# Performance work log

Measured on AMD Instinct MI355X. Metric: run time of the kernel, lower is better.

## Reference

```python
import jax, jax.numpy as jnp
import numpy as np


def setup_inputs() -> dict:
    key = jax.random.key(0)
    k1, k2, k3 = jax.random.split(key, 3)
    return {
        "x": jax.random.normal(k1, (1, 64, 28, 28), dtype=jnp.float32),
        "w1": jax.random.normal(k2, (128, 32, 3, 3, 2), dtype=jnp.float32),  # weights[0]
        "w2": jax.random.normal(k3, (64, 3, 2), dtype=jnp.float32),          # weights[1]
    }


def reference(x, w1, w2):
    # Stage 1: first unfold + einsum == depthwise size-3 conv along W (pad 1),
    # producing 2 taps (k) per channel.
    xr = x.reshape(64, 28, 28)                      # (j, m=H, n=W)
    xp = jnp.pad(xr, ((0, 0), (0, 0), (1, 1)))      # zero-pad W by 1
    # t3[j, m, i, n] = xp[j, m, n + i]  (i = kernel offset 0..2)
    t3 = jnp.stack([xp[:, :, i:i + 28] for i in range(3)], axis=2)  # (64,28,3,28)
    t4 = jnp.einsum('jmin,jik->jmnk', t3, w2)       # (64,28,28,2)

    # Stage 2: pairwise channel-sum 64 -> 32
    t5 = t4.reshape(32, 2, 28, 28, 2).sum(axis=1)   # (l=32, h=28, w=28, k=2)

    # Stage 3: the two remaining unfolds + final einsum == standard 3x3 conv,
    # pad 1, in_channels = (l,k) = 64, out_channels = 128.
    inp = jnp.transpose(t5, (0, 3, 1, 2)).reshape(1, 64, 28, 28)       # NCHW, C=(l,k)
    w = jnp.transpose(w1, (0, 1, 4, 2, 3)).reshape(128, 64, 3, 3)      # OIHW, I=(l,m)
    y = jax.lax.conv_general_dilated(
        inp, w, window_strides=(1, 1), padding=((1, 1), (1, 1)),
        dimension_numbers=('NCHW', 'OIHW', 'NCHW'))
    return y  # (1, 128, 28, 28)
```

## Files before the change

kernel.cpp:

```cpp
#include <hip/hip_runtime.h>
#include <hip/hip_bf16.h>

__global__ __launch_bounds__(256, 2) void fused_kernel(
    const float* __restrict__ x,
    const float* __restrict__ w1,
    const float* __restrict__ w2,
    float* __restrict__ y)
{
    __shared__ __align__(16) float sA[64 * 220];

    const int b     = blockIdx.x;
    const int opair = b / 7;
    const int band  = b % 7;
    const int tid   = threadIdx.x;

    const int l8      = tid & 7;
    const int strip   = tid >> 3;
    const bool act    = (strip < 28);
    const int sclp    = act ? strip : 0;
    const int oo      = sclp / 14;
    const int rem     = sclp % 14;
    const int rp      = rem / 7;
    const int st      = rem % 7;
    const int o       = opair * 2 + oo;

    float2 wreg[4][9];
    {
        const float* wb = w1 + o * 576 + l8 * 18;
        #pragma unroll
        for (int li = 0; li < 4; ++li)
            #pragma unroll
            for (int t = 0; t < 9; ++t)
                wreg[li][t] = *(const float2*)(wb + li * 144 + t * 2);
    }

    if (tid < 192) {
        const int l  = tid / 6;
        const int pr = tid % 6;
        const int m  = band * 4 + pr - 1;
        const int j0 = 2 * l;
        float* dst0 = &sA[(2 * l)     * 220 + pr * 36];
        float* dst1 = &sA[(2 * l + 1) * 220 + pr * 36];
        if (m < 0 || m > 27) {
            #pragma unroll
            for (int t = 0; t < 7; ++t) {
                ((float4*)dst0)[t] = make_float4(0.f, 0.f, 0.f, 0.f);
                ((float4*)dst1)[t] = make_float4(0.f, 0.f, 0.f, 0.f);
            }
            ((float2*)dst0)[14] = make_float2(0.f, 0.f);
            ((float2*)dst1)[14] = make_float2(0.f, 0.f);
        } else {
            const float* xr0 = x + (j0 * 28 + m) * 28;
            const float* xr1 = xr0 + 28 * 28;
            const float2 a0 = *(const float2*)(w2 + j0 * 6 + 0);
            const float2 a1 = *(const float2*)(w2 + j0 * 6 + 2);
            const float2 a2 = *(const float2*)(w2 + j0 * 6 + 4);
            const float2 b0 = *(const float2*)(w2 + j0 * 6 + 6);
            const float2 b1 = *(const float2*)(w2 + j0 * 6 + 8);
            const float2 b2 = *(const float2*)(w2 + j0 * 6 + 10);

            float4 pv0 = make_float4(0.f, 0.f, 0.f, 0.f);
            float4 pv1 = make_float4(0.f, 0.f, 0.f, 0.f);
            #pragma unroll
            for (int t = 0; t < 7; ++t) {
                float4 v0 = ((const float4*)xr0)[t];
                float4 v1 = ((const float4*)xr1)[t];
                float4 o0, o1;
                o0.x = a0.x * pv0.z + a1.x * pv0.w + a2.x * v0.x
                     + b0.x * pv1.z + b1.x * pv1.w + b2.x * v1.x;
                o0.y = a0.x * pv0.w + a1.x * v0.x + a2.x * v0.y
                     + b0.x * pv1.w + b1.x * v1.x + b2.x * v1.y;
                o0.z = a0.x * v0.x + a1.x * v0.y + a2.x * v0.z
                     + b0.x * v1.x + b1.x * v1.y + b2.x * v1.z;
                o0.w = a0.x * v0.y + a1.x * v0.z + a2.x * v0.w
                     + b0.x * v1.y + b1.x * v1.z + b2.x * v1.w;
                o1.x = a0.y * pv0.z + a1.y * pv0.w + a2.y * v0.x
                     + b0.y * pv1.z + b1.y * pv1.w + b2.y * v1.x;
                o1.y = a0.y * pv0.w + a1.y * v0.x + a2.y * v0.y
                     + b0.y * pv1.w + b1.y * v1.x + b2.y * v1.y;
                o1.z = a0.y * v0.x + a1.y * v0.y + a2.y * v0.z
                     + b0.y * v1.x + b1.y * v1.y + b2.y * v1.z;
                o1.w = a0.y * v0.y + a1.y * v0.z + a2.y * v0.w
                     + b0.y * v1.y + b1.y * v1.z + b2.y * v1.w;
                if (t == 0) { o0.x = 0.f; o1.x = 0.f; }
                ((float4*)dst0)[t] = o0;
                ((float4*)dst1)[t] = o1;
                pv0 = v0; pv1 = v1;
            }
            float t28_0 = a0.x * pv0.z + a1.x * pv0.w
                        + b0.x * pv1.z + b1.x * pv1.w;
            float t28_1 = a0.y * pv0.z + a1.y * pv0.w
                        + b0.y * pv1.z + b1.y * pv1.w;
            ((float2*)dst0)[14] = make_float2(t28_0, 0.f);
            ((float2*)dst1)[14] = make_float2(t28_1, 0.f);
        }
    }
    __syncthreads();

    float acc00 = 0.f, acc01 = 0.f, acc02 = 0.f, acc03 = 0.f;
    float acc10 = 0.f, acc11 = 0.f, acc12 = 0.f, acc13 = 0.f;

    #pragma unroll
    for (int li = 0; li < 4; ++li) {
        #pragma unroll
        for (int ch = 0; ch < 2; ++ch) {
            const int c = (l8 + li * 8) * 2 + ch;
            const float* sa = &sA[c * 220 + (rp * 2) * 36 + st * 4];
            #pragma unroll
            for (int q = 0; q < 4; ++q) {
                float4 t0 = *(const float4*)(sa + q * 36);
                float2 t1 = *(const float2*)(sa + q * 36 + 4);
                if (q < 3) {
                    float2 W0 = wreg[li][q * 3 + 0];
                    float2 W1 = wreg[li][q * 3 + 1];
                    float2 W2 = wreg[li][q * 3 + 2];
                    float wa  = ch ? W0.y : W0.x;
                    float wbv = ch ? W1.y : W1.x;
                    float wc  = ch ? W2.y : W2.x;
                    acc00 += wa * t0.x + wbv * t0.y + wc * t0.z;
                    acc01 += wa * t0.y + wbv * t0.z + wc * t0.w;
                    acc02 += wa * t0.z + wbv * t0.w + wc * t1.x;
                    acc03 += wa * t0.w + wbv * t1.x + wc * t1.y;
                }
                if (q >= 1) {
                    float2 W0 = wreg[li][(q - 1) * 3 + 0];
                    float2 W1 = wreg[li][(q - 1) * 3 + 1];
                    float2 W2 = wreg[li][(q - 1) * 3 + 2];
                    float wa  = ch ? W0.y : W0.x;
                    float wbv = ch ? W1.y : W1.x;
                    float wc  = ch ? W2.y : W2.x;
                    acc10 += wa * t0.x + wbv * t0.y + wc * t0.z;
                    acc11 += wa * t0.y + wbv * t0.z + wc * t0.w;
                    acc12 += wa * t0.z + wbv * t0.w + wc * t1.x;
                    acc13 += wa * t0.w + wbv * t1.x + wc * t1.y;
                }
            }
        }
    }

    #pragma unroll
    for (int m = 1; m <= 4; m <<= 1) {
        acc00 += __shfl_xor(acc00, m); acc01 += __shfl_xor(acc01, m);
        acc02 += __shfl_xor(acc02, m); acc03 += __shfl_xor(acc03, m);
        acc10 += __shfl_xor(acc10, m); acc11 += __shfl_xor(acc11, m);
        acc12 += __shfl_xor(acc12, m); acc13 += __shfl_xor(acc13, m);
    }

    if (act && l8 == 0) {
        const int R0 = band * 4 + rp * 2;
        float* yp = y + (o * 28 + R0) * 28 + st * 4;
        *(float4*)yp        = make_float4(acc00, acc01, acc02, acc03);
        *(float4*)(yp + 28) = make_float4(acc10, acc11, acc12, acc13);
    }
}

extern "C" void kernel_launch(void* const* d_in, const int* in_sizes, int n_in,
                              void* d_out, int out_size, void* d_ws, size_t ws_size,
                              hipStream_t stream) {
    const float* x  = (const float*)d_in[0];
    const float* w1 = (const float*)d_in[1];
    const float* w2 = (const float*)d_in[2];
    float* yout = (float*)d_out;

    fused_kernel<<<dim3(448), dim3(256), 0, stream>>>(x, w1, w2, yout);
}
```

Measured before the change: 13.99 us.

## Interleave channel pairs in shared memory and pack accumulators as float2

Stage-1 output now goes to shared memory with the two k-taps of each channel pair interleaved, using one 372-float slab per pair instead of two 220-float slabs. The conv loop loads three float4 per row to cover both channels and accumulates into float2 pairs, which allows packed FMA and halves the number of LDS instructions per row. Shared memory per block drops, and launch bounds are raised to 3 blocks per CU for more occupancy. The trade-off is more register pressure under the tighter bound and different bank access patterns.

```diff
diff --git a/kernel.cpp b/kernel.cpp
--- a/kernel.cpp
+++ b/kernel.cpp
@@ -1,13 +1,13 @@
 #include <hip/hip_runtime.h>
 #include <hip/hip_bf16.h>
 
-__global__ __launch_bounds__(256, 2) void fused_kernel(
+__global__ __launch_bounds__(256, 3) void fused_kernel(
     const float* __restrict__ x,
     const float* __restrict__ w1,
     const float* __restrict__ w2,
     float* __restrict__ y)
 {
-    __shared__ __align__(16) float sA[64 * 220];
+    __shared__ __align__(16) float sB[32 * 372];
 
     const int b     = blockIdx.x;
     const int opair = b / 7;
@@ -39,16 +39,11 @@
         const int pr = tid % 6;
         const int m  = band * 4 + pr - 1;
         const int j0 = 2 * l;
-        float* dst0 = &sA[(2 * l)     * 220 + pr * 36];
-        float* dst1 = &sA[(2 * l + 1) * 220 + pr * 36];
+        float* dst = &sB[l * 372 + pr * 60];
         if (m < 0 || m > 27) {
             #pragma unroll
-            for (int t = 0; t < 7; ++t) {
-                ((float4*)dst0)[t] = make_float4(0.f, 0.f, 0.f, 0.f);
-                ((float4*)dst1)[t] = make_float4(0.f, 0.f, 0.f, 0.f);
-            }
-            ((float2*)dst0)[14] = make_float2(0.f, 0.f);
-            ((float2*)dst1)[14] = make_float2(0.f, 0.f);
+            for (int t = 0; t < 15; ++t)
+                ((float4*)dst)[t] = make_float4(0.f, 0.f, 0.f, 0.f);
         } else {
             const float* xr0 = x + (j0 * 28 + m) * 28;
             const float* xr1 = xr0 + 28 * 28;
@@ -65,78 +60,86 @@
             for (int t = 0; t < 7; ++t) {
                 float4 v0 = ((const float4*)xr0)[t];
                 float4 v1 = ((const float4*)xr1)[t];
-                float4 o0, o1;
-                o0.x = a0.x * pv0.z + a1.x * pv0.w + a2.x * v0.x
-                     + b0.x * pv1.z + b1.x * pv1.w + b2.x * v1.x;
-                o0.y = a0.x * pv0.w + a1.x * v0.x + a2.x * v0.y
-                     + b0.x * pv1.w + b1.x * v1.x + b2.x * v1.y;
-                o0.z = a0.x * v0.x + a1.x * v0.y + a2.x * v0.z
-                     + b0.x * v1.x + b1.x * v1.y + b2.x * v1.z;
-                o0.w = a0.x * v0.y + a1.x * v0.z + a2.x * v0.w
-                     + b0.x * v1.y + b1.x * v1.z + b2.x * v1.w;
-                o1.x = a0.y * pv0.z + a1.y * pv0.w + a2.y * v0.x
-                     + b0.y * pv1.z + b1.y * pv1.w + b2.y * v1.x;
-                o1.y = a0.y * pv0.w + a1.y * v0.x + a2.y * v0.y
-                     + b0.y * pv1.w + b1.y * v1.x + b2.y * v1.y;
-                o1.z = a0.y * v0.x + a1.y * v0.y + a2.y * v0.z
-                     + b0.y * v1.x + b1.y * v1.y + b2.y * v1.z;
-                o1.w = a0.y * v0.y + a1.y * v0.z + a2.y * v0.w
-                     + b0.y * v1.y + b1.y * v1.z + b2.y * v1.w;
-                if (t == 0) { o0.x = 0.f; o1.x = 0.f; }
-                ((float4*)dst0)[t] = o0;
-                ((float4*)dst1)[t] = o1;
+                float o0x = a0.x*pv0.z + a1.x*pv0.w + a2.x*v0.x
+                          + b0.x*pv1.z + b1.x*pv1.w + b2.x*v1.x;
+                float o1x = a0.y*pv0.z + a1.y*pv0.w + a2.y*v0.x
+                          + b0.y*pv1.z + b1.y*pv1.w + b2.y*v1.x;
+                float o0y = a0.x*pv0.w + a1.x*v0.x + a2.x*v0.y
+                          + b0.x*pv1.w + b1.x*v1.x + b2.x*v1.y;
+                float o1y = a0.y*pv0.w + a1.y*v0.x + a2.y*v0.y
+                          + b0.y*pv1.w + b1.y*v1.x + b2.y*v1.y;
+                float o0z = a0.x*v0.x + a1.x*v0.y + a2.x*v0.z
+                          + b0.x*v1.x + b1.x*v1.y + b2.x*v1.z;
+                float o1z = a0.y*v0.x + a1.y*v0.y + a2.y*v0.z
+                          + b0.y*v1.x + b1.y*v1.y + b2.y*v1.z;
+                float o0w = a0.x*v0.y + a1.x*v0.z + a2.x*v0.w
+                          + b0.x*v1.y + b1.x*v1.z + b2.x*v1.w;
+                float o1w = a0.y*v0.y + a1.y*v0.z + a2.y*v0.w
+                          + b0.y*v1.y + b1.y*v1.z + b2.y*v1.w;
+                if (t == 0) { o0x = 0.f; o1x = 0.f; }
+                ((float4*)dst)[2*t]     = make_float4(o0x, o1x, o0y, o1y);
+                ((float4*)dst)[2*t + 1] = make_float4(o0z, o1z, o0w, o1w);
                 pv0 = v0; pv1 = v1;
             }
-            float t28_0 = a0.x * pv0.z + a1.x * pv0.w
-                        + b0.x * pv1.z + b1.x * pv1.w;
-            float t28_1 = a0.y * pv0.z + a1.y * pv0.w
-                        + b0.y * pv1.z + b1.y * pv1.w;
-            ((float2*)dst0)[14] = make_float2(t28_0, 0.f);
-            ((float2*)dst1)[14] = make_float2(t28_1, 0.f);
+            float t28_0 = a0.x*pv0.z + a1.x*pv0.w + b0.x*pv1.z + b1.x*pv1.w;
+            float t28_1 = a0.y*pv0.z + a1.y*pv0.w + b0.y*pv1.z + b1.y*pv1.w;
+            ((float4*)dst)[14] = make_float4(t28_0, t28_1, 0.f, 0.f);
         }
     }
     __syncthreads();
 
-    float acc00 = 0.f, acc01 = 0.f, acc02 = 0.f, acc03 = 0.f;
-    float acc10 = 0.f, acc11 = 0.f, acc12 = 0.f, acc13 = 0.f;
+    float2 A00 = {0,0}, A01 = {0,0}, A02 = {0,0}, A03 = {0,0};
+    float2 A10 = {0,0}, A11 = {0,0}, A12 = {0,0}, A13 = {0,0};
 
     #pragma unroll
     for (int li = 0; li < 4; ++li) {
+        const int l = l8 + li * 8;
+        const float* sa = &sB[l * 372 + (rp * 2) * 60 + st * 8];
         #pragma unroll
-        for (int ch = 0; ch < 2; ++ch) {
-            const int c = (l8 + li * 8) * 2 + ch;
-            const float* sa = &sA[c * 220 + (rp * 2) * 36 + st * 4];
-            #pragma unroll
-            for (int q = 0; q < 4; ++q) {
-                float4 t0 = *(const float4*)(sa + q * 36);
-                float2 t1 = *(const float2*)(sa + q * 36 + 4);
-                if (q < 3) {
-                    float2 W0 = wreg[li][q * 3 + 0];
-                    float2 W1 = wreg[li][q * 3 + 1];
-                    float2 W2 = wreg[li][q * 3 + 2];
-                    float wa  = ch ? W0.y : W0.x;
-                    float wbv = ch ? W1.y : W1.x;
-                    float wc  = ch ? W2.y : W2.x;
-                    acc00 += wa * t0.x + wbv * t0.y + wc * t0.z;
-                    acc01 += wa * t0.y + wbv * t0.z + wc * t0.w;
-                    acc02 += wa * t0.z + wbv * t0.w + wc * t1.x;
-                    acc03 += wa * t0.w + wbv * t1.x + wc * t1.y;
-                }
-                if (q >= 1) {
-                    float2 W0 = wreg[li][(q - 1) * 3 + 0];
-                    float2 W1 = wreg[li][(q - 1) * 3 + 1];
-                    float2 W2 = wreg[li][(q - 1) * 3 + 2];
-                    float wa  = ch ? W0.y : W0.x;
-                    float wbv = ch ? W1.y : W1.x;
-                    float wc  = ch ? W2.y : W2.x;
-                    acc10 += wa * t0.x + wbv * t0.y + wc * t0.z;
-                    acc11 += wa * t0.y + wbv * t0.z + wc * t0.w;
-                    acc12 += wa * t0.z + wbv * t0.w + wc * t1.x;
-                    acc13 += wa * t0.w + wbv * t1.x + wc * t1.y;
-                }
+        for (int q = 0; q < 4; ++q) {
+            const float* row = sa + q * 60;
+            float4 T0 = *(const float4*)(row);
+            float4 T1 = *(const float4*)(row + 4);
+            float4 T2 = *(const float4*)(row + 8);
+            float2 p0 = make_float2(T0.x, T0.y);
+            float2 p1 = make_float2(T0.z, T0.w);
+            float2 p2 = make_float2(T1.x, T1.y);
+            float2 p3 = make_float2(T1.z, T1.w);
+            float2 p4 = make_float2(T2.x, T2.y);
+            float2 p5 = make_float2(T2.z, T2.w);
+            if (q < 3) {
+                float2 W0 = wreg[li][q * 3 + 0];
+                float2 W1 = wreg[li][q * 3 + 1];
+                float2 W2 = wreg[li][q * 3 + 2];
+                A00.x += W0.x*p0.x + W1.x*p1.x + W2.x*p2.x;
+                A00.y += W0.y*p0.y + W1.y*p1.y + W2.y*p2.y;
+                A01.x += W0.x*p1.x + W1.x*p2.x + W2.x*p3.x;
+                A01.y += W0.y*p1.y + W1.y*p2.y + W2.y*p3.y;
+                A02.x += W0.x*p2.x + W1.x*p3.x + W2.x*p4.x;
+                A02.y += W0.y*p2.y + W1.y*p3.y + W2.y*p4.y;
+                A03.x += W0.x*p3.x + W1.x*p4.x + W2.x*p5.x;
+                A03.y += W0.y*p3.y + W1.y*p4.y + W2.y*p5.y;
+            }
+            if (q >= 1) {
+                float2 W0 = wreg[li][(q - 1) * 3 + 0];
+                float2 W1 = wreg[li][(q - 1) * 3 + 1];
+                float2 W2 = wreg[li][(q - 1) * 3 + 2];
+                A10.x += W0.x*p0.x + W1.x*p1.x + W2.x*p2.x;
+                A10.y += W0.y*p0.y + W1.y*p1.y + W2.y*p2.y;
+                A11.x += W0.x*p1.x + W1.x*p2.x + W2.x*p3.x;
+                A11.y += W0.y*p1.y + W1.y*p2.y + W2.y*p3.y;
+                A12.x += W0.x*p2.x + W1.x*p3.x + W2.x*p4.x;
+                A12.y += W0.y*p2.y + W1.y*p3.y + W2.y*p4.y;
+                A13.x += W0.x*p3.x + W1.x*p4.x + W2.x*p5.x;
+                A13.y += W0.y*p3.y + W1.y*p4.y + W2.y*p5.y;
             }
         }
     }
+
+    float acc00 = A00.x + A00.y, acc01 = A01.x + A01.y;
+    float acc02 = A02.x + A02.y, acc03 = A03.x + A03.y;
+    float acc10 = A10.x + A10.y, acc11 = A11.x + A11.y;
+    float acc12 = A12.x + A12.y, acc13 = A13.x + A13.y;
 
     #pragma unroll
     for (int m = 1; m <= 4; m <<= 1) {
```

Result: slower. 26.55 us (+89.8%).
